# Performance work log

Hardware: AMD Instinct MI355X
Metric: run time of the kernel (lower is better)

Reference implementation:

```python
import jax, jax.numpy as jnp
import numpy as np

H, B, T = 4, 16, 4000
E, D, A, C, K, O = 512, 512, 128, 10, 101, 512


def setup_inputs() -> dict:
    key = jax.random.key(0)
    ks = jax.random.split(key, 12)
    return {
        "enc_pad": jax.random.normal(ks[0], (B, T, E), jnp.float32),
        "enc_len": jax.random.randint(ks[1], (B,), T // 2, T + 1, jnp.int32),
        "dec_z": jax.random.normal(ks[2], (B, D), jnp.float32),
        "att_prev": jax.random.uniform(ks[3], (H, B, T), jnp.float32) / T,
        # learned parameters (per-head stacks)
        "Wenc": jax.random.normal(ks[4], (H, E, A), jnp.float32) / np.sqrt(E).astype(np.float32),
        "benc": jnp.zeros((H, A), jnp.float32),
        "Wdec": jax.random.normal(ks[5], (H, D, A), jnp.float32) / np.sqrt(D).astype(np.float32),
        "Watt": jax.random.normal(ks[6], (H, C, A), jnp.float32) / np.sqrt(C).astype(np.float32),
        "conv_w": jax.random.normal(ks[7], (H, C, K), jnp.float32) / np.sqrt(K).astype(np.float32),
        "gv": jax.random.normal(ks[8], (H, A), jnp.float32) / np.sqrt(A).astype(np.float32),
        "Wo": jax.random.normal(ks[9], (H * E, O), jnp.float32) / np.sqrt(H * E).astype(np.float32),
        "bo": jnp.zeros((O,), jnp.float32),
    }


def reference(enc_pad, enc_len, dec_z, att_prev, Wenc, benc, Wdec, Watt, conv_w, gv, Wo, bo):
    scaling = 1.0
    Hh, Bb, Tt = att_prev.shape
    Cc, Kk = conv_w.shape[1], conv_w.shape[2]
    pad_l = Kk // 2
    pad_r = Kk // 2 if Kk % 2 == 1 else Kk // 2 - 1
    # location conv: grouped 1D conv over heads. lhs [B,H,Tp], rhs [H*C,1,K]
    x = jnp.pad(att_prev.transpose(1, 0, 2), ((0, 0), (0, 0), (pad_l, pad_r)))
    rhs = conv_w.reshape(Hh * Cc, 1, Kk)
    conv = jax.lax.conv_general_dilated(
        x, rhs, window_strides=(1,), padding='VALID',
        dimension_numbers=('NCH', 'OIH', 'NCH'), feature_group_count=Hh)  # [B,H*C,T]
    conv = conv.reshape(Bb, Hh, Cc, Tt)
    att_conv = jnp.einsum('bhct,hca->bhta', conv, Watt)                    # mlp_att
    enc_proj = jnp.einsum('bte,hea->bhta', enc_pad, Wenc) + benc[None, :, None, :]  # mlp_enc
    dec_proj = jnp.einsum('bd,hda->bha', dec_z, Wdec)[:, :, None, :]       # mlp_dec
    e = jnp.einsum('bhta,ha->bht', jnp.tanh(enc_proj + dec_proj + att_conv), gv)  # gvec
    w = jax.nn.softmax(scaling * e, axis=-1)                               # [B,H,T]
    c = jnp.einsum('bht,bte->bhe', w, enc_pad).reshape(Bb, Hh * enc_pad.shape[-1])
    out = c @ Wo + bo                                                      # mlp_o
    return out, w.transpose(1, 0, 2)  # ws stacked as [H,B,T]
```

## Files before the change

### kernel.cpp

```cpp
#include <hip/hip_runtime.h>
#include <hip/hip_bf16.h>

#define H_ 4
#define B_ 16
#define T_ 4000
#define E_ 512
#define D_ 512
#define A_ 128
#define C_ 10
#define K_ 101
#define O_ 512
#define TC_ 50
#define CH_ (T_ / TC_)

typedef __attribute__((ext_vector_type(16))) float f32x16;
typedef __attribute__((ext_vector_type(8)))  short short8;

#define MFMA32(a, b, c) __builtin_amdgcn_mfma_f32_32x32x16_bf16(a, b, c, 0, 0, 0)

#define GLL16(gp, lp) __builtin_amdgcn_global_load_lds( \
    (const __attribute__((address_space(1))) unsigned int*)(gp), \
    (__attribute__((address_space(3))) unsigned int*)(lp), 16, 0, 0)

static __device__ __forceinline__ unsigned short f2bf(float x) {
  unsigned u = __float_as_uint(x);
  unsigned r = (u + 0x7FFFu + ((u >> 16) & 1u)) >> 16;
  return (unsigned short)r;
}
static __device__ __forceinline__ unsigned pk2(float a, float b) {
  return (unsigned)f2bf(a) | ((unsigned)f2bf(b) << 16);
}
static __device__ __forceinline__ unsigned pkcvt(float a, float b) {
  __hip_bfloat162 h2 = __float22bfloat162_rn(make_float2(a, b));
  unsigned u; __builtin_memcpy(&u, &h2, 4); return u;
}
static __device__ __forceinline__ uint4 packbf8(float4 f0, float4 f1) {
  uint4 u;
  u.x = pkcvt(f0.x, f0.y); u.y = pkcvt(f0.z, f0.w);
  u.z = pkcvt(f1.x, f1.y); u.w = pkcvt(f1.z, f1.w);
  return u;
}
static __device__ __forceinline__ f32x16 zero16() {
  f32x16 z;
#pragma unroll
  for (int i = 0; i < 16; ++i) z[i] = 0.f;
  return z;
}
static __device__ __forceinline__ float tanh_fast(float x) {
  return 1.0f - 2.0f / (__expf(2.0f * x) + 1.0f);
}
static __device__ __forceinline__ int swz32(int r, int ksg) {
  return (r >> 1) * 128 + (((((r & 1) << 2) | ksg) ^ ((r >> 1) & 7)) << 4);
}
static __device__ __forceinline__ int swzC(int r, int sl) {
  return r * 128 + ((sl ^ (r & 7)) << 4);
}

__global__ __launch_bounds__(256) void k_prep(const float* __restrict__ Wenc,
                                              const float* __restrict__ Watt,
                                              const float* __restrict__ dec_z,
                                              const float* __restrict__ Wdec,
                                              const float* __restrict__ benc,
                                              char* __restrict__ wbs,
                                              char* __restrict__ wattb,
                                              float* __restrict__ addv4) {
  const int bid = blockIdx.x;
  const int tid = threadIdx.x;
  if (bid < 128) {
    const int c = bid * 256 + tid;
    const int cc = c & 2047;
    const int kt = c >> 11;
    const int line = cc >> 3, sp = cc & 7;
    const int sraw = sp ^ (line & 7);
    const int n = line * 2 + (sraw >> 2);
    const int ksg = sraw & 3;
    const int h = n >> 7, a = n & 127;
    const int kb = kt * 32 + ksg * 8;
    uint4 u;
    u.x = pk2(Wenc[((size_t)h * E_ + kb + 0) * A_ + a], Wenc[((size_t)h * E_ + kb + 1) * A_ + a]);
    u.y = pk2(Wenc[((size_t)h * E_ + kb + 2) * A_ + a], Wenc[((size_t)h * E_ + kb + 3) * A_ + a]);
    u.z = pk2(Wenc[((size_t)h * E_ + kb + 4) * A_ + a], Wenc[((size_t)h * E_ + kb + 5) * A_ + a]);
    u.w = pk2(Wenc[((size_t)h * E_ + kb + 6) * A_ + a], Wenc[((size_t)h * E_ + kb + 7) * A_ + a]);
    ((uint4*)wbs)[c] = u;
  } else if (bid == 128) {
#pragma unroll
    for (int q = 0; q < 4; ++q) {
      const int cw = q * 256 + tid;
      const int h = cw >> 8, cc = cw & 255;
      const int line = cc >> 3, sp = cc & 7;
      const int sraw = sp ^ (line & 7);
      const int a = line * 4 + (sraw >> 1);
      const int s = sraw & 1;
      unsigned short v[8];
#pragma unroll
      for (int j = 0; j < 8; ++j) {
        const int k = s * 8 + j;
        v[j] = (k < C_) ? f2bf(Watt[((size_t)h * C_ + k) * A_ + a]) : (unsigned short)0;
      }
      uint4 u;
      u.x = (unsigned)v[0] | ((unsigned)v[1] << 16);
      u.y = (unsigned)v[2] | ((unsigned)v[3] << 16);
      u.z = (unsigned)v[4] | ((unsigned)v[5] << 16);
      u.w = (unsigned)v[6] | ((unsigned)v[7] << 16);
      ((uint4*)wattb)[cw] = u;
    }
  } else {
    const int idx = bid - 129;
    const int b = idx >> 3, h = (idx >> 1) & 3, ks = idx & 1;
    const int a = tid & 127, kh = tid >> 7;
    const int p = ks * 2 + kh;
    const int d0 = p * 128;
    const float* z = dec_z + (size_t)b * D_ + d0;
    const float* w = Wdec + ((size_t)h * D_ + d0) * A_ + a;
    float s = (p == 0) ? benc[h * A_ + a] : 0.f;
#pragma unroll 8
    for (int d = 0; d < 128; ++d) s += z[d] * w[(size_t)d * A_];
    addv4[(((size_t)p * B_ + b) * H_ + h) * A_ + a] = s;
  }
}

__global__ __launch_bounds__(256) void k_conv(const float* __restrict__ att_prev,
                                              const float* __restrict__ conv_w,
                                              char* __restrict__ convpad) {
  const int bh = blockIdx.x;
  const int b = bh / H_, h = bh % H_;
  const int t0 = blockIdx.y * 256;
  __shared__ float ap[256 + K_ - 1 + 3];
  __shared__ float cw[C_ * K_];
  const float* src = att_prev + ((size_t)h * B_ + b) * T_;
  for (int i = threadIdx.x; i < 256 + K_ - 1; i += 256) {
    int tt = t0 - (K_ / 2) + i;
    ap[i] = (tt >= 0 && tt < T_) ? src[tt] : 0.f;
  }
  for (int i = threadIdx.x; i < C_ * K_; i += 256) cw[i] = conv_w[(size_t)h * C_ * K_ + i];
  __syncthreads();
  const int t = t0 + threadIdx.x;
  if (t < T_) {
    float s[C_];
#pragma unroll
    for (int c = 0; c < C_; ++c) s[c] = 0.f;
    for (int k = 0; k < K_; ++k) {
      float apv = ap[threadIdx.x + k];
#pragma unroll
      for (int c = 0; c < C_; ++c) s[c] += cw[c * K_ + k] * apv;
    }
    uint4 u0, u1;
    u0.x = pk2(s[0], s[1]); u0.y = pk2(s[2], s[3]);
    u0.z = pk2(s[4], s[5]); u0.w = pk2(s[6], s[7]);
    u1.x = pk2(s[8], s[9]); u1.y = 0u; u1.z = 0u; u1.w = 0u;
    char* dst = convpad + (size_t)(b * T_ + t) * 128 + h * 32;
    *(uint4*)dst = u0;
    *(uint4*)(dst + 16) = u1;
  }
}

__global__ __launch_bounds__(512, 2) void k_fused_e_mfma(
    const float* __restrict__ enc,
    const char*  __restrict__ wbs,
    const char*  __restrict__ convpad,
    const char*  __restrict__ wattb,
    const float* __restrict__ addv4,
    const float* __restrict__ gv,
    float* __restrict__ e_out) {
  __shared__ char smem[81920];
  const int ABUF0o = 0, ABUF1o = 8192, BBUF0o = 16384, BBUF1o = 49152;
  const int tid = threadIdx.x;
  const int wv = tid >> 6;
  const int wh = wv & 3;
  const int wm = wv >> 2;
  const int lane = tid & 63;
  const int ln31 = lane & 31;
  const int hi = lane >> 5;
  const int m0 = blockIdx.x * 128;
  const unsigned b0 = (unsigned)m0 / 4000u;
  const unsigned b1 = (unsigned)(m0 + 127) / 4000u;

  f32x16 acc[2][4];
#pragma unroll
  for (int i = 0; i < 2; ++i)
#pragma unroll
    for (int j = 0; j < 4; ++j) acc[i][j] = zero16();

  const int srow = tid >> 2, sksg = tid & 3;
  const int stA = swz32(srow, sksg);
  const float* encRow = enc + (size_t)(m0 + srow) * E_ + sksg * 8;
  const int wbase = wv * 1024;
  const int lof = lane * 16;

  {
    float4 f0 = ((const float4*)encRow)[0];
    float4 f1 = ((const float4*)encRow)[1];
    *(uint4*)(smem + ABUF0o + stA) = packbf8(f0, f1);
#pragma unroll
    for (int it = 0; it < 4; ++it)
      GLL16(wbs + (size_t)it * 8192 + wbase + lof, smem + BBUF0o + it * 8192 + wbase);
  }
  __syncthreads();

  for (int kt = 0; kt < 16; ++kt) {
    const int cur = kt & 1;
    const char* Ab = smem + (cur ? ABUF1o : ABUF0o);
    const char* Bb = smem + (cur ? BBUF1o : BBUF0o);
    char* An = smem + (cur ? ABUF0o : ABUF1o);
    char* Bn = smem + (cur ? BBUF0o : BBUF1o);

    uint4 pk = {0, 0, 0, 0};
    uint4 rc0 = {0, 0, 0, 0}, rc1 = {0, 0, 0, 0};
    float av0s = 0.f, av1s = 0.f, gvv = 0.f;

    if (kt < 15) {
      const float* apk = encRow + (kt + 1) * 32;
      float4 f0 = ((const float4*)apk)[0];
      float4 f1 = ((const float4*)apk)[1];
      pk = packbf8(f0, f1);
#pragma unroll
      for (int it = 0; it < 4; ++it)
        GLL16(wbs + (size_t)(kt + 1) * 32768 + it * 8192 + wbase + lof,
              Bn + it * 8192 + wbase);
    } else {
      rc0 = *(const uint4*)(convpad + (size_t)(m0 + (tid >> 3)) * 128 + (tid & 7) * 16);
      rc1 = *(const uint4*)(convpad + (size_t)(m0 + ((tid + 512) >> 3)) * 128 + (tid & 7) * 16);
#pragma unroll
      for (int it = 0; it < 2; ++it)
        GLL16(wattb + (size_t)it * 8192 + wbase + lof, Bn + 16384 + it * 8192 + wbase);
      av0s = addv4[b0 * 512 + tid]        + addv4[8192 + b0 * 512 + tid]
           + addv4[16384 + b0 * 512 + tid] + addv4[24576 + b0 * 512 + tid];
      av1s = addv4[b1 * 512 + tid]        + addv4[8192 + b1 * 512 + tid]
           + addv4[16384 + b1 * 512 + tid] + addv4[24576 + b1 * 512 + tid];
      gvv = gv[tid];
    }

#pragma unroll
    for (int kc = 0; kc < 2; ++kc) {
      const int ksg = kc * 2 + hi;
      short8 a0 = *(const short8*)(Ab + swz32(wm * 64 + ln31, ksg));
      short8 a1 = *(const short8*)(Ab + swz32(wm * 64 + 32 + ln31, ksg));
#pragma unroll
      for (int ni = 0; ni < 4; ++ni) {
        const int n = wh * 128 + ni * 32 + ln31;
        short8 bfr = *(const short8*)(Bb + swz32(n, ksg));
        acc[0][ni] = MFMA32(a0, bfr, acc[0][ni]);
        acc[1][ni] = MFMA32(a1, bfr, acc[1][ni]);
      }
    }

    if (kt < 15) {
      *(uint4*)(An + stA) = pk;
    } else {
      *(uint4*)(Bn + swzC(tid >> 3, tid & 7)) = rc0;
      *(uint4*)(Bn + swzC((tid + 512) >> 3, tid & 7)) = rc1;
      ((float*)An)[tid] = av0s;
      ((float*)An)[512 + tid] = av1s;
      ((float*)An)[1024 + tid] = gvv;
    }
    __syncthreads();
  }

  {
    const char* AconvL = smem + BBUF0o;
    const char* WattL  = smem + BBUF0o + 16384;
    const int sl = wh * 2 + hi;
    short8 ac0 = *(const short8*)(AconvL + swzC(wm * 64 + ln31, sl));
    short8 ac1 = *(const short8*)(AconvL + swzC(wm * 64 + 32 + ln31, sl));
#pragma unroll
    for (int ni = 0; ni < 4; ++ni) {
      const int a = ni * 32 + ln31;
      short8 wf = *(const short8*)(WattL + wh * 4096 + (a >> 2) * 128 +
                                   (((((a & 3) << 1) | hi) ^ ((a >> 2) & 7)) << 4));
      acc[0][ni] = MFMA32(ac0, wf, acc[0][ni]);
      acc[1][ni] = MFMA32(ac1, wf, acc[1][ni]);
    }
  }

  {
    const float* An_f = (const float*)(smem + ABUF0o);
    float av0[4], av1[4], gvr[4];
#pragma unroll
    for (int ni = 0; ni < 4; ++ni) {
      const int a = wh * 128 + ni * 32 + ln31;
      av0[ni] = An_f[a];
      av1[ni] = An_f[512 + a];
      gvr[ni] = An_f[1024 + a];
    }
#pragma unroll
    for (int mi = 0; mi < 2; ++mi) {
#pragma unroll
      for (int reg = 0; reg < 16; ++reg) {
        const int rl = wm * 64 + mi * 32 + (reg & 3) + ((reg >> 2) << 3) + (hi << 2);
        const unsigned brow = (unsigned)(m0 + rl);
        const unsigned bb = brow / 4000u;
        const unsigned tt = brow - bb * 4000u;
        const int sel = (bb != b0);
        float rs = 0.f;
#pragma unroll
        for (int ni = 0; ni < 4; ++ni) {
          float s = acc[mi][ni][reg] + (sel ? av1[ni] : av0[ni]);
          rs += gvr[ni] * tanh_fast(s);
        }
        rs += __shfl_xor(rs, 1);
        rs += __shfl_xor(rs, 2);
        rs += __shfl_xor(rs, 4);
        rs += __shfl_xor(rs, 8);
        rs += __shfl_xor(rs, 16);
        if (ln31 == 0) e_out[((size_t)bb * H_ + wh) * T_ + tt] = rs;
      }
    }
  }
}

__global__ __launch_bounds__(256) void k_msum(const float* __restrict__ e_in,
                                              float2* __restrict__ msum) {
  const int bh = blockIdx.x;
  const float* er = e_in + (size_t)bh * T_;
  __shared__ float red[256];
  const int tid = threadIdx.x;
  float m = -1e30f;
  for (int t = tid; t < T_; t += 256) m = fmaxf(m, er[t]);
  red[tid] = m;
  __syncthreads();
  for (int s = 128; s > 0; s >>= 1) {
    if (tid < s) red[tid] = fmaxf(red[tid], red[tid + s]);
    __syncthreads();
  }
  m = red[0];
  __syncthreads();
  float sum = 0.f;
  for (int t = tid; t < T_; t += 256) sum += __expf(er[t] - m);
  red[tid] = sum;
  __syncthreads();
  for (int s = 128; s > 0; s >>= 1) {
    if (tid < s) red[tid] += red[tid + s];
    __syncthreads();
  }
  if (tid == 0) msum[bh] = make_float2(m, 1.0f / red[0]);
}

__global__ __launch_bounds__(128) void k_ctx(const float* __restrict__ enc,
                                             const float* __restrict__ e_in,
                                             const float2* __restrict__ msum,
                                             float* __restrict__ wout,
                                             float* __restrict__ partial) {
  const int b = blockIdx.x, tc = blockIdx.y;
  const int t0 = tc * CH_;
  const int tid = threadIdx.x;
  __shared__ float wls[H_ * CH_];
  for (int i = tid; i < H_ * CH_; i += 128) {
    const int h = i / CH_, tt = i - h * CH_;
    const float2 ms = msum[b * H_ + h];
    const float w = __expf(e_in[((size_t)b * H_ + h) * T_ + t0 + tt] - ms.x) * ms.y;
    wls[i] = w;
    wout[((size_t)h * B_ + b) * T_ + t0 + tt] = w;
  }
  __syncthreads();
  float4 a0 = {0,0,0,0}, a1 = {0,0,0,0}, a2 = {0,0,0,0}, a3 = {0,0,0,0};
  const float4* enc4 = (const float4*)enc;
  const size_t ebase = ((size_t)b * T_ + t0) * 128 + tid;
#pragma unroll 4
  for (int tt = 0; tt < CH_; ++tt) {
    const float4 x = enc4[ebase + (size_t)tt * 128];
    const float w0 = wls[tt], w1 = wls[CH_ + tt], w2 = wls[2 * CH_ + tt], w3 = wls[3 * CH_ + tt];
    a0.x += w0 * x.x; a0.y += w0 * x.y; a0.z += w0 * x.z; a0.w += w0 * x.w;
    a1.x += w1 * x.x; a1.y += w1 * x.y; a1.z += w1 * x.z; a1.w += w1 * x.w;
    a2.x += w2 * x.x; a2.y += w2 * x.y; a2.z += w2 * x.z; a2.w += w2 * x.w;
    a3.x += w3 * x.x; a3.y += w3 * x.y; a3.z += w3 * x.z; a3.w += w3 * x.w;
  }
  float4* p4 = (float4*)partial;
  const size_t pbase = (((size_t)tc * B_ + b) * H_) * 128 + tid;
  p4[pbase] = a0;
  p4[pbase + 128] = a1;
  p4[pbase + 256] = a2;
  p4[pbase + 384] = a3;
}

__global__ __launch_bounds__(256) void k_out_part(const float* __restrict__ partial,
                                                  const float* __restrict__ Wo,
                                                  float* __restrict__ p2) {
  const int b = blockIdx.x;
  const int o = blockIdx.y * 256 + threadIdx.x;
  const int kc = blockIdx.z;
  __shared__ float cS[256];
  const int he0 = kc * 256;
  {
    float s = 0.f;
#pragma unroll
    for (int tc = 0; tc < TC_; ++tc)
      s += partial[((size_t)tc * B_ + b) * (H_ * E_) + he0 + threadIdx.x];
    cS[threadIdx.x] = s;
  }
  __syncthreads();
  float s = 0.f;
#pragma unroll 8
  for (int i = 0; i < 256; ++i) s += cS[i] * Wo[(size_t)(he0 + i) * O_ + o];
  p2[((size_t)kc * B_ + b) * O_ + o] = s;
}

__global__ __launch_bounds__(512) void k_out_fin(const float* __restrict__ p2,
                                                 const float* __restrict__ bo,
                                                 float* __restrict__ out) {
  const int b = blockIdx.x, o = threadIdx.x;
  float s = bo[o];
#pragma unroll
  for (int kc = 0; kc < 8; ++kc) s += p2[((size_t)kc * B_ + b) * O_ + o];
  out[b * O_ + o] = s;
}

extern "C" void kernel_launch(void* const* d_in, const int* in_sizes, int n_in,
                              void* d_out, int out_size, void* d_ws, size_t ws_size,
                              hipStream_t stream) {
  (void)in_sizes; (void)n_in; (void)out_size; (void)ws_size;
  const float* enc      = (const float*)d_in[0];
  const float* dec_z    = (const float*)d_in[2];
  const float* att_prev = (const float*)d_in[3];
  const float* Wenc     = (const float*)d_in[4];
  const float* benc     = (const float*)d_in[5];
  const float* Wdec     = (const float*)d_in[6];
  const float* Watt     = (const float*)d_in[7];
  const float* conv_w   = (const float*)d_in[8];
  const float* gv       = (const float*)d_in[9];
  const float* Wo       = (const float*)d_in[10];
  const float* bo       = (const float*)d_in[11];

  float* out  = (float*)d_out;
  float* wout = out + B_ * O_;

  char* wsb = (char*)d_ws;
  float*  e_buf   = (float*)(wsb);
  char*   convpad = wsb + 1024000;
  char*   wbs     = wsb + 9216000;
  char*   wattb   = wsb + 9740288;
  float*  addv4   = (float*)(wsb + 9756672);
  float2* msum    = (float2*)(wsb + 9887744);
  float*  partial = (float*)(wsb + 9888256);
  float*  p2      = (float*)(wsb + 16441856);

  hipLaunchKernelGGL(k_prep, dim3(257), dim3(256), 0, stream,
                     Wenc, Watt, dec_z, Wdec, benc, wbs, wattb, addv4);
  hipLaunchKernelGGL(k_conv, dim3(B_ * H_, 16), dim3(256), 0, stream, att_prev, conv_w, convpad);
  hipLaunchKernelGGL(k_fused_e_mfma, dim3(500), dim3(512), 0, stream,
                     enc, wbs, convpad, wattb, addv4, gv, e_buf);
  hipLaunchKernelGGL(k_msum, dim3(B_ * H_), dim3(256), 0, stream, e_buf, msum);
  hipLaunchKernelGGL(k_ctx, dim3(B_, TC_), dim3(128), 0, stream, enc, e_buf, msum, wout, partial);
  hipLaunchKernelGGL(k_out_part, dim3(B_, O_ / 256, 8), dim3(256), 0, stream, partial, Wo, p2);
  hipLaunchKernelGGL(k_out_fin, dim3(B_), dim3(512), 0, stream, p2, bo, out);
}
```

Measured before the change: 148.5 us.

## Prefetch encoder tile two steps ahead with explicit vmcnt waits in GEMM loop

```diff
diff --git a/kernel.cpp b/kernel.cpp
--- a/kernel.cpp
+++ b/kernel.cpp
@@ -187,16 +187,24 @@
   const int wbase = wv * 1024;
   const int lof = lane * 16;
 
-  {
-    float4 f0 = ((const float4*)encRow)[0];
-    float4 f1 = ((const float4*)encRow)[1];
-    *(uint4*)(smem + ABUF0o + stA) = packbf8(f0, f1);
-#pragma unroll
-    for (int it = 0; it < 4; ++it)
-      GLL16(wbs + (size_t)it * 8192 + wbase + lof, smem + BBUF0o + it * 8192 + wbase);
-  }
-  __syncthreads();
-
+#pragma unroll
+  for (int it = 0; it < 4; ++it)
+    GLL16(wbs + (size_t)it * 8192 + wbase + lof, smem + BBUF0o + it * 8192 + wbase);
+  __builtin_amdgcn_sched_barrier(0);
+  float4 cF0 = ((const float4*)encRow)[0];
+  float4 cF1 = ((const float4*)encRow)[1];
+  float4 nF0 = ((const float4*)(encRow + 32))[0];
+  float4 nF1 = ((const float4*)(encRow + 32))[1];
+  *(uint4*)(smem + ABUF0o + stA) = packbf8(cF0, cF1);
+  cF0 = nF0; cF1 = nF1;
+  asm volatile("s_waitcnt vmcnt(2) lgkmcnt(0)" ::: "memory");
+  __builtin_amdgcn_sched_barrier(0);
+  __builtin_amdgcn_s_barrier();
+
+  uint4 rc0 = {0, 0, 0, 0}, rc1 = {0, 0, 0, 0};
+  float av0s = 0.f, av1s = 0.f, gvv = 0.f;
+
+#pragma unroll
   for (int kt = 0; kt < 16; ++kt) {
     const int cur = kt & 1;
     const char* Ab = smem + (cur ? ABUF1o : ABUF0o);
@@ -204,25 +212,25 @@
     char* An = smem + (cur ? ABUF0o : ABUF1o);
     char* Bn = smem + (cur ? BBUF0o : BBUF1o);
 
-    uint4 pk = {0, 0, 0, 0};
-    uint4 rc0 = {0, 0, 0, 0}, rc1 = {0, 0, 0, 0};
-    float av0s = 0.f, av1s = 0.f, gvv = 0.f;
-
     if (kt < 15) {
-      const float* apk = encRow + (kt + 1) * 32;
-      float4 f0 = ((const float4*)apk)[0];
-      float4 f1 = ((const float4*)apk)[1];
-      pk = packbf8(f0, f1);
 #pragma unroll
       for (int it = 0; it < 4; ++it)
         GLL16(wbs + (size_t)(kt + 1) * 32768 + it * 8192 + wbase + lof,
               Bn + it * 8192 + wbase);
     } else {
+#pragma unroll
+      for (int it = 0; it < 2; ++it)
+        GLL16(wattb + (size_t)it * 8192 + wbase + lof, Bn + 16384 + it * 8192 + wbase);
+    }
+    __builtin_amdgcn_sched_barrier(0);
+
+    if (kt < 14) {
+      nF0 = ((const float4*)(encRow + (kt + 2) * 32))[0];
+      nF1 = ((const float4*)(encRow + (kt + 2) * 32))[1];
+    }
+    if (kt == 15) {
       rc0 = *(const uint4*)(convpad + (size_t)(m0 + (tid >> 3)) * 128 + (tid & 7) * 16);
       rc1 = *(const uint4*)(convpad + (size_t)(m0 + ((tid + 512) >> 3)) * 128 + (tid & 7) * 16);
-#pragma unroll
-      for (int it = 0; it < 2; ++it)
-        GLL16(wattb + (size_t)it * 8192 + wbase + lof, Bn + 16384 + it * 8192 + wbase);
       av0s = addv4[b0 * 512 + tid]        + addv4[8192 + b0 * 512 + tid]
            + addv4[16384 + b0 * 512 + tid] + addv4[24576 + b0 * 512 + tid];
       av1s = addv4[b1 * 512 + tid]        + addv4[8192 + b1 * 512 + tid]
@@ -245,7 +253,8 @@
     }
 
     if (kt < 15) {
-      *(uint4*)(An + stA) = pk;
+      *(uint4*)(An + stA) = packbf8(cF0, cF1);
+      cF0 = nF0; cF1 = nF1;
     } else {
       *(uint4*)(Bn + swzC(tid >> 3, tid & 7)) = rc0;
       *(uint4*)(Bn + swzC((tid + 512) >> 3, tid & 7)) = rc1;
@@ -253,7 +262,14 @@
       ((float*)An)[512 + tid] = av1s;
       ((float*)An)[1024 + tid] = gvv;
     }
-    __syncthreads();
+
+    if (kt < 14) {
+      asm volatile("s_waitcnt vmcnt(2) lgkmcnt(0)" ::: "memory");
+    } else {
+      asm volatile("s_waitcnt vmcnt(0) lgkmcnt(0)" ::: "memory");
+    }
+    __builtin_amdgcn_sched_barrier(0);
+    __builtin_amdgcn_s_barrier();
   }
 
   {
@@ -355,7 +371,7 @@
   float4 a0 = {0,0,0,0}, a1 = {0,0,0,0}, a2 = {0,0,0,0}, a3 = {0,0,0,0};
   const float4* enc4 = (const float4*)enc;
   const size_t ebase = ((size_t)b * T_ + t0) * 128 + tid;
-#pragma unroll 4
+#pragma unroll 8
   for (int tt = 0; tt < CH_; ++tt) {
     const float4 x = enc4[ebase + (size_t)tt * 128];
     const float w0 = wls[tt], w1 = wls[CH_ + tt], w2 = wls[2 * CH_ + tt], w3 = wls[3 * CH_ + tt];
```

Result: faster. 145.5 us (-2.0%).

## Software-pipeline the fused MFMA GEMM loop with explicit waitcnt barriers and register prefetch

Applied to the files above, without the earlier changes.

```diff
diff --git a/kernel.cpp b/kernel.cpp
--- a/kernel.cpp
+++ b/kernel.cpp
@@ -30,14 +30,15 @@
 static __device__ __forceinline__ unsigned pk2(float a, float b) {
   return (unsigned)f2bf(a) | ((unsigned)f2bf(b) << 16);
 }
-static __device__ __forceinline__ unsigned pkcvt(float a, float b) {
-  __hip_bfloat162 h2 = __float22bfloat162_rn(make_float2(a, b));
-  unsigned u; __builtin_memcpy(&u, &h2, 4); return u;
+static __device__ __forceinline__ unsigned cvtpk(float lo, float hi) {
+  unsigned r;
+  asm("v_cvt_pk_bf16_f32 %0, %1, %2" : "=v"(r) : "v"(lo), "v"(hi));
+  return r;
 }
 static __device__ __forceinline__ uint4 packbf8(float4 f0, float4 f1) {
   uint4 u;
-  u.x = pkcvt(f0.x, f0.y); u.y = pkcvt(f0.z, f0.w);
-  u.z = pkcvt(f1.x, f1.y); u.w = pkcvt(f1.z, f1.w);
+  u.x = cvtpk(f0.x, f0.y); u.y = cvtpk(f0.z, f0.w);
+  u.z = cvtpk(f1.x, f1.y); u.w = cvtpk(f1.z, f1.w);
   return u;
 }
 static __device__ __forceinline__ f32x16 zero16() {
@@ -163,7 +164,6 @@
     const float* __restrict__ gv,
     float* __restrict__ e_out) {
   __shared__ char smem[81920];
-  const int ABUF0o = 0, ABUF1o = 8192, BBUF0o = 16384, BBUF1o = 49152;
   const int tid = threadIdx.x;
   const int wv = tid >> 6;
   const int wh = wv & 3;
@@ -182,83 +182,125 @@
     for (int j = 0; j < 4; ++j) acc[i][j] = zero16();
 
   const int srow = tid >> 2, sksg = tid & 3;
-  const int stA = swz32(srow, sksg);
-  const float* encRow = enc + (size_t)(m0 + srow) * E_ + sksg * 8;
-  const int wbase = wv * 1024;
-  const int lof = lane * 16;
-
+  char* wrA = smem + swz32(srow, sksg);
+  const float* encP = enc + (size_t)(m0 + srow) * E_ + sksg * 8;
+  const char* wp = wbs + wv * 1024 + lane * 16;
+  char* gllB1 = smem + 49152 + wv * 1024;
+  char* gllB0 = smem + 16384 + wv * 1024;
+  const int aoff = swz32(wm * 64 + ln31, hi);
+  const int boff = swz32(wh * 128 + ln31, hi);
+  const char* pA  = smem + aoff;
+  const char* pAx = smem + (aoff ^ 32);
+  const char* pB  = smem + 16384 + boff;
+  const char* pBx = smem + 16384 + (boff ^ 32);
+
+#define MSTEP(AOFF, BOFF) do {                                                  \
+    { short8 a0_ = *(const short8*)(pA + (AOFF));                               \
+      short8 a1_ = *(const short8*)(pA + (AOFF) + 2048);                        \
+      short8 b_;                                                                \
+      b_ = *(const short8*)(pB + (BOFF));                                       \
+      acc[0][0] = MFMA32(a0_, b_, acc[0][0]); acc[1][0] = MFMA32(a1_, b_, acc[1][0]); \
+      b_ = *(const short8*)(pB + (BOFF) + 2048);                                \
+      acc[0][1] = MFMA32(a0_, b_, acc[0][1]); acc[1][1] = MFMA32(a1_, b_, acc[1][1]); \
+      b_ = *(const short8*)(pB + (BOFF) + 4096);                                \
+      acc[0][2] = MFMA32(a0_, b_, acc[0][2]); acc[1][2] = MFMA32(a1_, b_, acc[1][2]); \
+      b_ = *(const short8*)(pB + (BOFF) + 6144);                                \
+      acc[0][3] = MFMA32(a0_, b_, acc[0][3]); acc[1][3] = MFMA32(a1_, b_, acc[1][3]); } \
+    { short8 a0_ = *(const short8*)(pAx + (AOFF));                              \
+      short8 a1_ = *(const short8*)(pAx + (AOFF) + 2048);                       \
+      short8 b_;                                                                \
+      b_ = *(const short8*)(pBx + (BOFF));                                      \
+      acc[0][0] = MFMA32(a0_, b_, acc[0][0]); acc[1][0] = MFMA32(a1_, b_, acc[1][0]); \
+      b_ = *(const short8*)(pBx + (BOFF) + 2048);                               \
+      acc[0][1] = MFMA32(a0_, b_, acc[0][1]); acc[1][1] = MFMA32(a1_, b_, acc[1][1]); \
+      b_ = *(const short8*)(pBx + (BOFF) + 4096);                               \
+      acc[0][2] = MFMA32(a0_, b_, acc[0][2]); acc[1][2] = MFMA32(a1_, b_, acc[1][2]); \
+      b_ = *(const short8*)(pBx + (BOFF) + 6144);                               \
+      acc[0][3] = MFMA32(a0_, b_, acc[0][3]); acc[1][3] = MFMA32(a1_, b_, acc[1][3]); } \
+  } while (0)
+
+#define CBAR(N) do {                                                            \
+    asm volatile("s_waitcnt vmcnt(" #N ") lgkmcnt(0)" ::: "memory");            \
+    __builtin_amdgcn_sched_barrier(0);                                          \
+    __builtin_amdgcn_s_barrier();                                               \
+  } while (0)
+
+  float4 rA0, rA1, rB0, rB1;
+
+#pragma unroll
+  for (int it = 0; it < 4; ++it)
+    GLL16(wp + it * 8192, gllB0 + it * 8192);
+  __builtin_amdgcn_sched_barrier(0);
   {
-    float4 f0 = ((const float4*)encRow)[0];
-    float4 f1 = ((const float4*)encRow)[1];
-    *(uint4*)(smem + ABUF0o + stA) = packbf8(f0, f1);
+    float4 t0 = ((const float4*)encP)[0];
+    float4 t1 = ((const float4*)encP)[1];
+    rA0 = ((const float4*)(encP + 32))[0];
+    rA1 = ((const float4*)(encP + 32))[1];
+    *(uint4*)wrA = packbf8(t0, t1);
+  }
+  encP += 64;
+  wp += 32768;
+  CBAR(2);
+
+#pragma unroll 1
+  for (int ktp = 0; ktp < 7; ++ktp) {
 #pragma unroll
     for (int it = 0; it < 4; ++it)
-      GLL16(wbs + (size_t)it * 8192 + wbase + lof, smem + BBUF0o + it * 8192 + wbase);
-  }
-  __syncthreads();
-
-  for (int kt = 0; kt < 16; ++kt) {
-    const int cur = kt & 1;
-    const char* Ab = smem + (cur ? ABUF1o : ABUF0o);
-    const char* Bb = smem + (cur ? BBUF1o : BBUF0o);
-    char* An = smem + (cur ? ABUF0o : ABUF1o);
-    char* Bn = smem + (cur ? BBUF0o : BBUF1o);
-
-    uint4 pk = {0, 0, 0, 0};
-    uint4 rc0 = {0, 0, 0, 0}, rc1 = {0, 0, 0, 0};
-    float av0s = 0.f, av1s = 0.f, gvv = 0.f;
-
-    if (kt < 15) {
-      const float* apk = encRow + (kt + 1) * 32;
-      float4 f0 = ((const float4*)apk)[0];
-      float4 f1 = ((const float4*)apk)[1];
-      pk = packbf8(f0, f1);
-#pragma unroll
-      for (int it = 0; it < 4; ++it)
-        GLL16(wbs + (size_t)(kt + 1) * 32768 + it * 8192 + wbase + lof,
-              Bn + it * 8192 + wbase);
-    } else {
-      rc0 = *(const uint4*)(convpad + (size_t)(m0 + (tid >> 3)) * 128 + (tid & 7) * 16);
-      rc1 = *(const uint4*)(convpad + (size_t)(m0 + ((tid + 512) >> 3)) * 128 + (tid & 7) * 16);
-#pragma unroll
-      for (int it = 0; it < 2; ++it)
-        GLL16(wattb + (size_t)it * 8192 + wbase + lof, Bn + 16384 + it * 8192 + wbase);
-      av0s = addv4[b0 * 512 + tid]        + addv4[8192 + b0 * 512 + tid]
-           + addv4[16384 + b0 * 512 + tid] + addv4[24576 + b0 * 512 + tid];
-      av1s = addv4[b1 * 512 + tid]        + addv4[8192 + b1 * 512 + tid]
-           + addv4[16384 + b1 * 512 + tid] + addv4[24576 + b1 * 512 + tid];
-      gvv = gv[tid];
-    }
-
-#pragma unroll
-    for (int kc = 0; kc < 2; ++kc) {
-      const int ksg = kc * 2 + hi;
-      short8 a0 = *(const short8*)(Ab + swz32(wm * 64 + ln31, ksg));
-      short8 a1 = *(const short8*)(Ab + swz32(wm * 64 + 32 + ln31, ksg));
-#pragma unroll
-      for (int ni = 0; ni < 4; ++ni) {
-        const int n = wh * 128 + ni * 32 + ln31;
-        short8 bfr = *(const short8*)(Bb + swz32(n, ksg));
-        acc[0][ni] = MFMA32(a0, bfr, acc[0][ni]);
-        acc[1][ni] = MFMA32(a1, bfr, acc[1][ni]);
-      }
-    }
-
-    if (kt < 15) {
-      *(uint4*)(An + stA) = pk;
-    } else {
-      *(uint4*)(Bn + swzC(tid >> 3, tid & 7)) = rc0;
-      *(uint4*)(Bn + swzC((tid + 512) >> 3, tid & 7)) = rc1;
-      ((float*)An)[tid] = av0s;
-      ((float*)An)[512 + tid] = av1s;
-      ((float*)An)[1024 + tid] = gvv;
-    }
-    __syncthreads();
-  }
+      GLL16(wp + it * 8192, gllB1 + it * 8192);
+    __builtin_amdgcn_sched_barrier(0);
+    rB0 = ((const float4*)encP)[0];
+    rB1 = ((const float4*)encP)[1];
+    __builtin_amdgcn_sched_barrier(0);
+    MSTEP(0, 0);
+    *(uint4*)(wrA + 8192) = packbf8(rA0, rA1);
+    encP += 32; wp += 32768;
+    CBAR(2);
+#pragma unroll
+    for (int it = 0; it < 4; ++it)
+      GLL16(wp + it * 8192, gllB0 + it * 8192);
+    __builtin_amdgcn_sched_barrier(0);
+    rA0 = ((const float4*)encP)[0];
+    rA1 = ((const float4*)encP)[1];
+    __builtin_amdgcn_sched_barrier(0);
+    MSTEP(8192, 32768);
+    *(uint4*)wrA = packbf8(rB0, rB1);
+    encP += 32; wp += 32768;
+    CBAR(2);
+  }
+
+#pragma unroll
+  for (int it = 0; it < 4; ++it)
+    GLL16(wp + it * 8192, gllB1 + it * 8192);
+  __builtin_amdgcn_sched_barrier(0);
+  MSTEP(0, 0);
+  *(uint4*)(wrA + 8192) = packbf8(rA0, rA1);
+  CBAR(0);
 
   {
-    const char* AconvL = smem + BBUF0o;
-    const char* WattL  = smem + BBUF0o + 16384;
+#pragma unroll
+    for (int it = 0; it < 2; ++it)
+      GLL16(wattb + (size_t)it * 8192 + wv * 1024 + lane * 16, gllB0 + 16384 + it * 8192);
+    __builtin_amdgcn_sched_barrier(0);
+    uint4 rc0 = *(const uint4*)(convpad + (size_t)(m0 + (tid >> 3)) * 128 + (tid & 7) * 16);
+    uint4 rc1 = *(const uint4*)(convpad + (size_t)(m0 + ((tid + 512) >> 3)) * 128 + (tid & 7) * 16);
+    float av0s = addv4[b0 * 512 + tid]         + addv4[8192 + b0 * 512 + tid]
+               + addv4[16384 + b0 * 512 + tid] + addv4[24576 + b0 * 512 + tid];
+    float av1s = addv4[b1 * 512 + tid]         + addv4[8192 + b1 * 512 + tid]
+               + addv4[16384 + b1 * 512 + tid] + addv4[24576 + b1 * 512 + tid];
+    float gvv = gv[tid];
+    __builtin_amdgcn_sched_barrier(0);
+    MSTEP(8192, 32768);
+    *(uint4*)(smem + 16384 + swzC(tid >> 3, tid & 7)) = rc0;
+    *(uint4*)(smem + 16384 + swzC((tid + 512) >> 3, tid & 7)) = rc1;
+    ((float*)smem)[tid] = av0s;
+    ((float*)smem)[512 + tid] = av1s;
+    ((float*)smem)[1024 + tid] = gvv;
+    CBAR(0);
+  }
+
+  {
+    const char* AconvL = smem + 16384;
+    const char* WattL  = smem + 32768;
     const int sl = wh * 2 + hi;
     short8 ac0 = *(const short8*)(AconvL + swzC(wm * 64 + ln31, sl));
     short8 ac1 = *(const short8*)(AconvL + swzC(wm * 64 + 32 + ln31, sl));
@@ -273,7 +315,7 @@
   }
 
   {
-    const float* An_f = (const float*)(smem + ABUF0o);
+    const float* An_f = (const float*)smem;
     float av0[4], av1[4], gvr[4];
 #pragma unroll
     for (int ni = 0; ni < 4; ++ni) {
@@ -306,6 +348,8 @@
       }
     }
   }
+#undef MSTEP
+#undef CBAR
 }
 
 __global__ __launch_bounds__(256) void k_msum(const float* __restrict__ e_in,
@@ -355,7 +399,7 @@
   float4 a0 = {0,0,0,0}, a1 = {0,0,0,0}, a2 = {0,0,0,0}, a3 = {0,0,0,0};
   const float4* enc4 = (const float4*)enc;
   const size_t ebase = ((size_t)b * T_ + t0) * 128 + tid;
-#pragma unroll 4
+#pragma unroll 8
   for (int tt = 0; tt < CH_; ++tt) {
     const float4 x = enc4[ebase + (size_t)tt * 128];
     const float w0 = wls[tt], w1 = wls[CH_ + tt], w2 = wls[2 * CH_ + tt], w3 = wls[3 * CH_ + tt];
```

Measured after the change: 143.4 us. 1.04x faster.

## Restructure fused score kernel per head with resident LDS weights and register-fed A

Applied to the files above, without the earlier changes.

```diff
diff --git a/kernel.cpp b/kernel.cpp
--- a/kernel.cpp
+++ b/kernel.cpp
@@ -30,15 +30,18 @@
 static __device__ __forceinline__ unsigned pk2(float a, float b) {
   return (unsigned)f2bf(a) | ((unsigned)f2bf(b) << 16);
 }
-static __device__ __forceinline__ unsigned pkcvt(float a, float b) {
-  __hip_bfloat162 h2 = __float22bfloat162_rn(make_float2(a, b));
-  unsigned u; __builtin_memcpy(&u, &h2, 4); return u;
-}
-static __device__ __forceinline__ uint4 packbf8(float4 f0, float4 f1) {
+static __device__ __forceinline__ unsigned cvtpk(float lo, float hi) {
+  unsigned r;
+  asm("v_cvt_pk_bf16_f32 %0, %1, %2" : "=v"(r) : "v"(lo), "v"(hi));
+  return r;
+}
+static __device__ __forceinline__ short8 pack8(float4 a, float4 b) {
   uint4 u;
-  u.x = pkcvt(f0.x, f0.y); u.y = pkcvt(f0.z, f0.w);
-  u.z = pkcvt(f1.x, f1.y); u.w = pkcvt(f1.z, f1.w);
-  return u;
+  u.x = cvtpk(a.x, a.y); u.y = cvtpk(a.z, a.w);
+  u.z = cvtpk(b.x, b.y); u.w = cvtpk(b.z, b.w);
+  short8 r;
+  __builtin_memcpy(&r, &u, 16);
+  return r;
 }
 static __device__ __forceinline__ f32x16 zero16() {
   f32x16 z;
@@ -51,9 +54,6 @@
 }
 static __device__ __forceinline__ int swz32(int r, int ksg) {
   return (r >> 1) * 128 + (((((r & 1) << 2) | ksg) ^ ((r >> 1) & 7)) << 4);
-}
-static __device__ __forceinline__ int swzC(int r, int sl) {
-  return r * 128 + ((sl ^ (r & 7)) << 4);
 }
 
 __global__ __launch_bounds__(256) void k_prep(const float* __restrict__ Wenc,
@@ -162,18 +162,14 @@
     const float* __restrict__ addv4,
     const float* __restrict__ gv,
     float* __restrict__ e_out) {
-  __shared__ char smem[81920];
-  const int ABUF0o = 0, ABUF1o = 8192, BBUF0o = 16384, BBUF1o = 49152;
+  __shared__ char smem[135168];
   const int tid = threadIdx.x;
   const int wv = tid >> 6;
-  const int wh = wv & 3;
-  const int wm = wv >> 2;
   const int lane = tid & 63;
   const int ln31 = lane & 31;
   const int hi = lane >> 5;
-  const int m0 = blockIdx.x * 128;
-  const unsigned b0 = (unsigned)m0 / 4000u;
-  const unsigned b1 = (unsigned)(m0 + 127) / 4000u;
+  const int h = blockIdx.x & 3;
+  const int m0 = (blockIdx.x >> 2) * 512;
 
   f32x16 acc[2][4];
 #pragma unroll
@@ -181,116 +177,96 @@
 #pragma unroll
     for (int j = 0; j < 4; ++j) acc[i][j] = zero16();
 
-  const int srow = tid >> 2, sksg = tid & 3;
-  const int stA = swz32(srow, sksg);
-  const float* encRow = enc + (size_t)(m0 + srow) * E_ + sksg * 8;
-  const int wbase = wv * 1024;
-  const int lof = lane * 16;
+#pragma unroll
+  for (int kt = 0; kt < 16; ++kt)
+    GLL16(wbs + (size_t)kt * 32768 + h * 8192 + wv * 1024 + lane * 16,
+          smem + kt * 8192 + wv * 1024);
+  if (wv < 4)
+    GLL16(wattb + h * 4096 + wv * 1024 + lane * 16, smem + 131072 + wv * 1024);
+
+  const int r0 = m0 + wv * 64 + ln31;
+  const int r1 = r0 + 32;
+  const float* eR0 = enc + (size_t)r0 * E_ + hi * 8;
+  const float* eR1 = enc + (size_t)r1 * E_ + hi * 8;
+  int boff[4];
+#pragma unroll
+  for (int ni = 0; ni < 4; ++ni) boff[ni] = swz32(ni * 32 + ln31, hi);
+
+  float4 f00 = ((const float4*)eR0)[0];
+  float4 f01 = ((const float4*)eR0)[1];
+  float4 f02 = ((const float4*)eR0)[4];
+  float4 f03 = ((const float4*)eR0)[5];
+  float4 f10 = ((const float4*)eR1)[0];
+  float4 f11 = ((const float4*)eR1)[1];
+  float4 f12 = ((const float4*)eR1)[4];
+  float4 f13 = ((const float4*)eR1)[5];
+
+  __syncthreads();
+
+#pragma unroll 2
+  for (int kt = 0; kt < 16; ++kt) {
+    short8 a00 = pack8(f00, f01);
+    short8 a01 = pack8(f02, f03);
+    short8 a10 = pack8(f10, f11);
+    short8 a11 = pack8(f12, f13);
+    if (kt < 15) {
+      const float4* p0 = (const float4*)eR0 + (kt + 1) * 8;
+      const float4* p1 = (const float4*)eR1 + (kt + 1) * 8;
+      f00 = p0[0]; f01 = p0[1]; f02 = p0[4]; f03 = p0[5];
+      f10 = p1[0]; f11 = p1[1]; f12 = p1[4]; f13 = p1[5];
+    }
+    const char* pB = smem + kt * 8192;
+#pragma unroll
+    for (int ni = 0; ni < 4; ++ni) {
+      short8 b0_ = *(const short8*)(pB + boff[ni]);
+      acc[0][ni] = MFMA32(a00, b0_, acc[0][ni]);
+      acc[1][ni] = MFMA32(a10, b0_, acc[1][ni]);
+    }
+#pragma unroll
+    for (int ni = 0; ni < 4; ++ni) {
+      short8 b1_ = *(const short8*)(pB + (boff[ni] ^ 32));
+      acc[0][ni] = MFMA32(a01, b1_, acc[0][ni]);
+      acc[1][ni] = MFMA32(a11, b1_, acc[1][ni]);
+    }
+  }
 
   {
-    float4 f0 = ((const float4*)encRow)[0];
-    float4 f1 = ((const float4*)encRow)[1];
-    *(uint4*)(smem + ABUF0o + stA) = packbf8(f0, f1);
-#pragma unroll
-    for (int it = 0; it < 4; ++it)
-      GLL16(wbs + (size_t)it * 8192 + wbase + lof, smem + BBUF0o + it * 8192 + wbase);
-  }
-  __syncthreads();
-
-  for (int kt = 0; kt < 16; ++kt) {
-    const int cur = kt & 1;
-    const char* Ab = smem + (cur ? ABUF1o : ABUF0o);
-    const char* Bb = smem + (cur ? BBUF1o : BBUF0o);
-    char* An = smem + (cur ? ABUF0o : ABUF1o);
-    char* Bn = smem + (cur ? BBUF0o : BBUF1o);
-
-    uint4 pk = {0, 0, 0, 0};
-    uint4 rc0 = {0, 0, 0, 0}, rc1 = {0, 0, 0, 0};
-    float av0s = 0.f, av1s = 0.f, gvv = 0.f;
-
-    if (kt < 15) {
-      const float* apk = encRow + (kt + 1) * 32;
-      float4 f0 = ((const float4*)apk)[0];
-      float4 f1 = ((const float4*)apk)[1];
-      pk = packbf8(f0, f1);
-#pragma unroll
-      for (int it = 0; it < 4; ++it)
-        GLL16(wbs + (size_t)(kt + 1) * 32768 + it * 8192 + wbase + lof,
-              Bn + it * 8192 + wbase);
-    } else {
-      rc0 = *(const uint4*)(convpad + (size_t)(m0 + (tid >> 3)) * 128 + (tid & 7) * 16);
-      rc1 = *(const uint4*)(convpad + (size_t)(m0 + ((tid + 512) >> 3)) * 128 + (tid & 7) * 16);
-#pragma unroll
-      for (int it = 0; it < 2; ++it)
-        GLL16(wattb + (size_t)it * 8192 + wbase + lof, Bn + 16384 + it * 8192 + wbase);
-      av0s = addv4[b0 * 512 + tid]        + addv4[8192 + b0 * 512 + tid]
-           + addv4[16384 + b0 * 512 + tid] + addv4[24576 + b0 * 512 + tid];
-      av1s = addv4[b1 * 512 + tid]        + addv4[8192 + b1 * 512 + tid]
-           + addv4[16384 + b1 * 512 + tid] + addv4[24576 + b1 * 512 + tid];
-      gvv = gv[tid];
-    }
-
-#pragma unroll
-    for (int kc = 0; kc < 2; ++kc) {
-      const int ksg = kc * 2 + hi;
-      short8 a0 = *(const short8*)(Ab + swz32(wm * 64 + ln31, ksg));
-      short8 a1 = *(const short8*)(Ab + swz32(wm * 64 + 32 + ln31, ksg));
-#pragma unroll
-      for (int ni = 0; ni < 4; ++ni) {
-        const int n = wh * 128 + ni * 32 + ln31;
-        short8 bfr = *(const short8*)(Bb + swz32(n, ksg));
-        acc[0][ni] = MFMA32(a0, bfr, acc[0][ni]);
-        acc[1][ni] = MFMA32(a1, bfr, acc[1][ni]);
-      }
-    }
-
-    if (kt < 15) {
-      *(uint4*)(An + stA) = pk;
-    } else {
-      *(uint4*)(Bn + swzC(tid >> 3, tid & 7)) = rc0;
-      *(uint4*)(Bn + swzC((tid + 512) >> 3, tid & 7)) = rc1;
-      ((float*)An)[tid] = av0s;
-      ((float*)An)[512 + tid] = av1s;
-      ((float*)An)[1024 + tid] = gvv;
-    }
-    __syncthreads();
+    short8 c0 = *(const short8*)(convpad + (size_t)r0 * 128 + h * 32 + hi * 16);
+    short8 c1 = *(const short8*)(convpad + (size_t)r1 * 128 + h * 32 + hi * 16);
+    const char* WattL = smem + 131072;
+#pragma unroll
+    for (int ni = 0; ni < 4; ++ni) {
+      const int ar = ni * 32 + ln31;
+      short8 wf = *(const short8*)(WattL + (ar >> 2) * 128 +
+                                   (((((ar & 3) << 1) | hi) ^ ((ar >> 2) & 7)) << 4));
+      acc[0][ni] = MFMA32(c0, wf, acc[0][ni]);
+      acc[1][ni] = MFMA32(c1, wf, acc[1][ni]);
+    }
   }
 
   {
-    const char* AconvL = smem + BBUF0o;
-    const char* WattL  = smem + BBUF0o + 16384;
-    const int sl = wh * 2 + hi;
-    short8 ac0 = *(const short8*)(AconvL + swzC(wm * 64 + ln31, sl));
-    short8 ac1 = *(const short8*)(AconvL + swzC(wm * 64 + 32 + ln31, sl));
+    const int wr0 = m0 + wv * 64;
+    const unsigned b0w = (unsigned)wr0 / 4000u;
+    const unsigned b1w = (unsigned)(wr0 + 63) / 4000u;
+    float av0[4], av1[4], gvr[4];
 #pragma unroll
     for (int ni = 0; ni < 4; ++ni) {
       const int a = ni * 32 + ln31;
-      short8 wf = *(const short8*)(WattL + wh * 4096 + (a >> 2) * 128 +
-                                   (((((a & 3) << 1) | hi) ^ ((a >> 2) & 7)) << 4));
-      acc[0][ni] = MFMA32(ac0, wf, acc[0][ni]);
-      acc[1][ni] = MFMA32(ac1, wf, acc[1][ni]);
-    }
-  }
-
-  {
-    const float* An_f = (const float*)(smem + ABUF0o);
-    float av0[4], av1[4], gvr[4];
-#pragma unroll
-    for (int ni = 0; ni < 4; ++ni) {
-      const int a = wh * 128 + ni * 32 + ln31;
-      av0[ni] = An_f[a];
-      av1[ni] = An_f[512 + a];
-      gvr[ni] = An_f[1024 + a];
+      const int i0 = (int)b0w * 512 + h * 128 + a;
+      const int i1 = (int)b1w * 512 + h * 128 + a;
+      av0[ni] = addv4[i0] + addv4[8192 + i0] + addv4[16384 + i0] + addv4[24576 + i0];
+      av1[ni] = addv4[i1] + addv4[8192 + i1] + addv4[16384 + i1] + addv4[24576 + i1];
+      gvr[ni] = gv[h * 128 + a];
     }
 #pragma unroll
     for (int mi = 0; mi < 2; ++mi) {
 #pragma unroll
       for (int reg = 0; reg < 16; ++reg) {
-        const int rl = wm * 64 + mi * 32 + (reg & 3) + ((reg >> 2) << 3) + (hi << 2);
-        const unsigned brow = (unsigned)(m0 + rl);
+        const int rl = mi * 32 + (reg & 3) + ((reg >> 2) << 3) + (hi << 2);
+        const unsigned brow = (unsigned)(wr0 + rl);
         const unsigned bb = brow / 4000u;
         const unsigned tt = brow - bb * 4000u;
-        const int sel = (bb != b0);
+        const int sel = (bb != b0w);
         float rs = 0.f;
 #pragma unroll
         for (int ni = 0; ni < 4; ++ni) {
@@ -302,7 +278,7 @@
         rs += __shfl_xor(rs, 4);
         rs += __shfl_xor(rs, 8);
         rs += __shfl_xor(rs, 16);
-        if (ln31 == 0) e_out[((size_t)bb * H_ + wh) * T_ + tt] = rs;
+        if (ln31 == 0) e_out[((size_t)bb * H_ + h) * T_ + tt] = rs;
       }
     }
   }
@@ -355,7 +331,7 @@
   float4 a0 = {0,0,0,0}, a1 = {0,0,0,0}, a2 = {0,0,0,0}, a3 = {0,0,0,0};
   const float4* enc4 = (const float4*)enc;
   const size_t ebase = ((size_t)b * T_ + t0) * 128 + tid;
-#pragma unroll 4
+#pragma unroll 8
   for (int tt = 0; tt < CH_; ++tt) {
     const float4 x = enc4[ebase + (size_t)tt * 128];
     const float w0 = wls[tt], w1 = wls[CH_ + tt], w2 = wls[2 * CH_ + tt], w3 = wls[3 * CH_ + tt];
```

New measurement: 183.0 us. 1.23x slower.
